# Kernel optimization log

Measured on AMD Instinct MI355X. Metric: run time of the kernel, lower is better.

## Reference

```python
import jax, jax.numpy as jnp
import numpy as np

B, T = 2048, 2048
VOCAB, E, H = 32000, 4, 4


def _gru_layer(x, Wih, Whh, bih, bhh, reverse=False):
    """PyTorch-semantics GRU over batch_first x [B,T,F]; returns [B,T,H]."""
    Bn = x.shape[0]
    Hn = Whh.shape[1]
    # Precompute input projections for all timesteps: [B,T,3H]
    xi = jnp.einsum('btf,gf->btg', x, Wih) + bih
    if reverse:
        xi = xi[:, ::-1]
    xi_t = jnp.swapaxes(xi, 0, 1)  # [T,B,3H]

    def step(h, xt):
        gh = h @ Whh.T + bhh                      # [B,3H]
        xr, xz, xn = jnp.split(xt, 3, axis=-1)
        hr, hz, hn = jnp.split(gh, 3, axis=-1)
        r = jax.nn.sigmoid(xr + hr)
        z = jax.nn.sigmoid(xz + hz)
        n = jnp.tanh(xn + r * hn)
        h_new = (1.0 - z) * n + z * h
        return h_new, h_new

    h0 = jnp.zeros((Bn, Hn), x.dtype)
    _, ys = jax.lax.scan(step, h0, xi_t)
    ys = jnp.swapaxes(ys, 0, 1)  # [B,T,H]
    if reverse:
        ys = ys[:, ::-1]
    return ys


def setup_inputs() -> dict:
    key = jax.random.key(0)
    ks = jax.random.split(key, 16)
    x = jax.random.randint(ks[0], (B, T), 0, VOCAB, dtype=jnp.int64)
    s = 0.3  # xavier-ish scale for tiny dims
    emb   = jax.random.normal(ks[1], (VOCAB, E), jnp.float32) * s
    Wih_f = jax.random.normal(ks[2], (3 * H, E), jnp.float32) * s
    Whh_f = jax.random.normal(ks[3], (3 * H, H), jnp.float32) * s
    Wih_b = jax.random.normal(ks[4], (3 * H, E), jnp.float32) * s
    Whh_b = jax.random.normal(ks[5], (3 * H, H), jnp.float32) * s
    Wih_o = jax.random.normal(ks[6], (3 * 1, 2 * H), jnp.float32) * s
    Whh_o = jax.random.normal(ks[7], (3 * 1, 1), jnp.float32) * s
    z = jnp.zeros
    return {
        'x': x, 'emb': emb,
        'Wih_f': Wih_f, 'Whh_f': Whh_f, 'bih_f': z((3 * H,)), 'bhh_f': z((3 * H,)),
        'Wih_b': Wih_b, 'Whh_b': Whh_b, 'bih_b': z((3 * H,)), 'bhh_b': z((3 * H,)),
        'Wih_o': Wih_o, 'Whh_o': Whh_o, 'bih_o': z((3,)), 'bhh_o': z((3,)),
    }


def reference(x, emb, Wih_f, Whh_f, bih_f, bhh_f, Wih_b, Whh_b, bih_b, bhh_b,
              Wih_o, Whh_o, bih_o, bhh_o):
    h = emb[x]                                         # [B,T,E]
    fwd = _gru_layer(h, Wih_f, Whh_f, bih_f, bhh_f, reverse=False)
    bwd = _gru_layer(h, Wih_b, Whh_b, bih_b, bhh_b, reverse=True)
    bi = jnp.concatenate([fwd, bwd], axis=-1)          # [B,T,2H]
    out = _gru_layer(bi, Wih_o, Whh_o, bih_o, bhh_o)   # [B,T,1]
    return jax.nn.sigmoid(out).reshape(x.shape[0], -1) # [B,T]
```

## Files before the change

kernel.cpp:

```cpp
#include <hip/hip_runtime.h>
#include <hip/hip_bf16.h>
#include <hip/hip_fp16.h>


#define NB 2048
#define NT 2048
#define NV 32000
#define PA_CH 32
#define PA_CL 64
#define PA_WUP 24
#define PB_CH 64
#define PB_CL 32
#define PB_WUP 16
#define CH 32
#define CL (NT / CH)
#define WUP 64

#define W_EMB    0
#define W_WIH_F  128000
#define W_WHH_F  128048
#define W_BIH_F  128096
#define W_BHH_F  128108
#define W_WIH_B  128120
#define W_WHH_B  128168
#define W_BIH_B  128216
#define W_BHH_B  128228
#define W_WIH_O  128240
#define W_WHH_O  128264
#define W_BIH_O  128267
#define W_BHH_O  128270
#define W_TOTAL  128273

#define XT_PAD 24

static constexpr size_t WBLK_BYTES = 524288;
static constexpr size_t D_BYTES    = (size_t)NT * NB * 8;
static constexpr size_t XT_BYTES_P = (size_t)(NT + 2 * XT_PAD) * NB * 2;
static constexpr size_t XIH_BYTES  = (size_t)NV * 16 * 2;
static constexpr size_t N2_XIH_F   = WBLK_BYTES;
static constexpr size_t N2_XIH_B   = N2_XIH_F + XIH_BYTES;
static constexpr size_t N2_DF      = N2_XIH_B + XIH_BYTES;
static constexpr size_t N2_DB      = N2_DF + D_BYTES;
static constexpr size_t N2_XT      = N2_DB + D_BYTES;
static constexpr size_t NEED_NEW2  = N2_XT + XT_BYTES_P;
static constexpr size_t XI_STRIDE  = 16;
static constexpr size_t XI_BYTES   = (size_t)NV * XI_STRIDE * 4;
static constexpr size_t HS_BYTES   = (size_t)NT * NB * 4 * 2;
static constexpr size_t OFF_XI_F   = WBLK_BYTES;
static constexpr size_t OFF_XI_B   = OFF_XI_F + XI_BYTES;
static constexpr size_t OFF_HS_B   = OFF_XI_B + XI_BYTES;
static constexpr size_t OFF_HS_F   = OFF_HS_B + HS_BYTES;
static constexpr size_t NEED_XI    = OFF_HS_B;
static constexpr size_t NEED_FAST  = OFF_HS_F + HS_BYTES;

#define L2E  1.4426950408889634f
#define L2E2 2.8853900817779268f

typedef __attribute__((ext_vector_type(2))) _Float16 h2v;

__device__ __forceinline__ float frcp_(float x) { return __builtin_amdgcn_rcpf(x); }
__device__ __forceinline__ float sigm_(float x) { return frcp_(1.f + __expf(-x)); }
__device__ __forceinline__ float tanh_(float x) { return 1.f - 2.f * frcp_(1.f + __expf(2.f * x)); }
__device__ __forceinline__ float b2f_(__hip_bfloat16 v) { return __bfloat162float(v); }
__device__ __forceinline__ unsigned f2bf_(float f) {
  __hip_bfloat16 h = __float2bfloat16(f);
  return (unsigned)__builtin_bit_cast(unsigned short, h);
}
__device__ __forceinline__ unsigned pack2_(float a, float b) { return f2bf_(a) | (f2bf_(b) << 16); }
__device__ __forceinline__ float bflo_(unsigned u) { return __builtin_bit_cast(float, u << 16); }
__device__ __forceinline__ float bfhi_(unsigned u) { return __builtin_bit_cast(float, u & 0xffff0000u); }
__device__ __forceinline__ float2 h2f2_(unsigned u) {
  __half2 h = __builtin_bit_cast(__half2, u);
  return __half22float2(h);
}
__device__ __forceinline__ unsigned packh2_(float a, float b) {
  __half2 h = __floats2half2_rn(a, b);
  return __builtin_bit_cast(unsigned, h);
}
__device__ __forceinline__ h2v packh2v_(float a, float b) {
  return __builtin_bit_cast(h2v, packh2_(a, b));
}

#if __has_builtin(__builtin_amdgcn_fdot2)
#define FDOT2_(a, b, c) __builtin_amdgcn_fdot2((a), (b), (c), false)
#else
__device__ __forceinline__ float FDOT2_(h2v a, h2v b, float c) {
  return c + (float)a.x * (float)b.x + (float)a.y * (float)b.y;
}
#endif
#if __has_builtin(__builtin_amdgcn_exp2f)
#define EXP2_(x) __builtin_amdgcn_exp2f(x)
#else
#define EXP2_(x) __expf(0.6931471805599453f * (x))
#endif

__device__ __forceinline__ int probe_is_bf16_(const void* emb) {
  const unsigned short* u = (const unsigned short*)emb;
  int sane = 0;
#pragma unroll
  for (int i = 0; i < 64; ++i) {
    unsigned short v = u[2 * i];
    unsigned e = (v >> 7) & 0xff;
    sane += (e >= 107 && e <= 146) || ((v & 0x7fff) == 0);
  }
  return sane >= 48;
}
__device__ __forceinline__ int probe_x_is64_(const int* x) {
  int zeros = 0;
#pragma unroll
  for (int i = 0; i < 32; ++i) zeros += (x[2 * i + 1] == 0);
  return zeros >= 28;
}
__device__ __forceinline__ int tok_(const int* x, size_t idx, int is64) {
  return is64 ? x[idx * 2] : x[idx];
}
__device__ __forceinline__ float ldf_(const void* p, int i, int isb) {
  return isb ? b2f_(((const __hip_bfloat16*)p)[i]) : ((const float*)p)[i];
}

__global__ void prep_p10(const int* __restrict__ x,
                         const void* emb, const void* Wih_f, const void* Whh_f,
                         const void* bih_f, const void* bhh_f,
                         const void* Wih_b, const void* Whh_b,
                         const void* bih_b, const void* bhh_b,
                         const void* Wih_o, const void* Whh_o,
                         const void* bih_o, const void* bhh_o,
                         __half* __restrict__ xih_f, __half* __restrict__ xih_b,
                         unsigned short* __restrict__ xT, float* __restrict__ W) {
  __shared__ int tile[64][65];
  const int blk = blockIdx.x;
  if (blk < 251) {
    const int tid = blk * 256 + (int)threadIdx.x;
    if (tid >= 2 * NV) return;
    const int isb = probe_is_bf16_(emb);
    const int dir = (tid >= NV) ? 1 : 0;
    const int v = dir ? tid - NV : tid;
    const void* Wih = dir ? Wih_b : Wih_f;
    const void* bih = dir ? bih_b : bih_f;
    const void* bhh = dir ? bhh_b : bhh_f;
    char* dst = (char*)((dir ? xih_b : xih_f) + (size_t)v * 16);
    const float e0 = ldf_(emb, v * 4 + 0, isb), e1 = ldf_(emb, v * 4 + 1, isb);
    const float e2 = ldf_(emb, v * 4 + 2, isb), e3 = ldf_(emb, v * 4 + 3, isb);
    float g[12];
#pragma unroll
    for (int gi = 0; gi < 12; ++gi) {
      float s = ldf_(bih, gi, isb) + (gi < 8 ? ldf_(bhh, gi, isb) : 0.f);
      s += ldf_(Wih, gi * 4 + 0, isb) * e0 + ldf_(Wih, gi * 4 + 1, isb) * e1 +
           ldf_(Wih, gi * 4 + 2, isb) * e2 + ldf_(Wih, gi * 4 + 3, isb) * e3;
      g[gi] = s * (gi < 8 ? L2E : L2E2);
    }
    uint4 qa, qb;
    qa.x = packh2_(g[0], g[1]);  qa.y = packh2_(g[2], g[3]);
    qa.z = packh2_(g[4], g[5]);  qa.w = packh2_(g[6], g[7]);
    qb.x = packh2_(g[8], g[9]);  qb.y = packh2_(g[10], g[11]);
    qb.z = 0u; qb.w = 0u;
    *(uint4*)(dst) = qa;
    *(uint4*)(dst + 16) = qb;
  } else if (blk < 1275) {
    const int x64 = probe_x_is64_(x);
    const int bi2 = blk - 251;
    const int tb = bi2 & 31;
    const int tt = bi2 >> 5;
    const int b0 = tb * 64, t0 = tt * 64;
    const int r = (int)threadIdx.x >> 2;
    const int s = (int)threadIdx.x & 3;
    const int bb = b0 + r;
    if (x64) {
      const uint4* p = (const uint4*)(x + ((size_t)bb * NT + t0 + s * 16) * 2);
#pragma unroll
      for (int i = 0; i < 8; ++i) {
        uint4 q = p[i];
        tile[r][s * 16 + 2 * i] = (int)q.x;
        tile[r][s * 16 + 2 * i + 1] = (int)q.z;
      }
    } else {
      const uint4* p = (const uint4*)(x + (size_t)bb * NT + t0 + s * 16);
#pragma unroll
      for (int i = 0; i < 4; ++i) {
        uint4 q = p[i];
        const int base = s * 16 + 4 * i;
        tile[r][base] = (int)q.x; tile[r][base + 1] = (int)q.y;
        tile[r][base + 2] = (int)q.z; tile[r][base + 3] = (int)q.w;
      }
    }
    __syncthreads();
    const int tx = (int)threadIdx.x & 63, ty = (int)threadIdx.x >> 6;
#pragma unroll
    for (int j = 0; j < 16; ++j) {
      const int t = t0 + ty + 4 * j;
      xT[(size_t)t * NB + b0 + tx] = (unsigned short)tile[tx][ty + 4 * j];
    }
  } else {
    const int i0 = (int)threadIdx.x;
    if (i0 >= W_TOTAL - W_WHH_F) return;
    const int isb = probe_is_bf16_(emb);
    const int i = W_WHH_F + i0;
    const void* src; int off;
    if      (i < W_BIH_F) { src = Whh_f; off = i - W_WHH_F; }
    else if (i < W_BHH_F) { src = bih_f; off = i - W_BIH_F; }
    else if (i < W_WIH_B) { src = bhh_f; off = i - W_BHH_F; }
    else if (i < W_WHH_B) { src = Wih_b; off = i - W_WIH_B; }
    else if (i < W_BIH_B) { src = Whh_b; off = i - W_WHH_B; }
    else if (i < W_BHH_B) { src = bih_b; off = i - W_BIH_B; }
    else if (i < W_WIH_O) { src = bhh_b; off = i - W_BHH_B; }
    else if (i < W_WHH_O) { src = Wih_o; off = i - W_WIH_O; }
    else if (i < W_BIH_O) { src = Whh_o; off = i - W_WHH_O; }
    else if (i < W_BHH_O) { src = bih_o; off = i - W_BIH_O; }
    else                  { src = bhh_o; off = i - W_BHH_O; }
    W[i] = ldf_(src, off, isb);
  }
}

__global__ void __launch_bounds__(64, 2)
gru_scan_p10(const unsigned short* __restrict__ xT, const float* __restrict__ W,
             const __half* __restrict__ xih_f, const __half* __restrict__ xih_b,
             unsigned* __restrict__ df, unsigned* __restrict__ db) {
  const int bi = blockIdx.x;
  const int rg = bi & 31;
  const int c = (bi >> 5) & (PA_CH - 1);
  const int dir = bi >> 10;
  const int b = rg * 64 + (int)threadIdx.x;
  const char* __restrict__ xib = (const char*)(dir ? xih_b : xih_f);
  const char* __restrict__ xtb = (const char*)xT;
  char* __restrict__ dsb = (char*)(dir ? db : df);
  const float* Whh = W + (dir ? W_WHH_B : W_WHH_F);
  const float* bhh = W + (dir ? W_BHH_B : W_BHH_F);

  h2v wh01[12], wh23[12];
#pragma unroll
  for (int g = 0; g < 12; ++g) {
    const float sc = (g < 8) ? L2E : L2E2;
    wh01[g] = packh2v_(Whh[g * 4 + 0] * sc, Whh[g * 4 + 1] * sc);
    wh23[g] = packh2v_(Whh[g * 4 + 2] * sc, Whh[g * 4 + 3] * sc);
  }
  float bn[4];
#pragma unroll
  for (int j = 0; j < 4; ++j) bn[j] = bhh[8 + j] * L2E2;
  h2v wr01 = packh2v_(W[W_WIH_O + dir * 4 + 0] * L2E, W[W_WIH_O + dir * 4 + 1] * L2E);
  h2v wr23 = packh2v_(W[W_WIH_O + dir * 4 + 2] * L2E, W[W_WIH_O + dir * 4 + 3] * L2E);
  h2v wz01 = packh2v_(W[W_WIH_O + 8 + dir * 4 + 0] * L2E, W[W_WIH_O + 8 + dir * 4 + 1] * L2E);
  h2v wz23 = packh2v_(W[W_WIH_O + 8 + dir * 4 + 2] * L2E, W[W_WIH_O + 8 + dir * 4 + 3] * L2E);
  h2v wn01 = packh2v_(W[W_WIH_O + 16 + dir * 4 + 0] * L2E2, W[W_WIH_O + 16 + dir * 4 + 1] * L2E2);
  h2v wn23 = packh2v_(W[W_WIH_O + 16 + dir * 4 + 2] * L2E2, W[W_WIH_O + 16 + dir * 4 + 3] * L2E2);

  const int lo = c * PA_CL, hi = lo + PA_CL;
  int t0, d, wsteps;
  if (dir == 0) {
    d = 1;
    t0 = (c == 0) ? 0 : lo - PA_WUP;
    wsteps = (c == 0) ? 0 : PA_WUP;
  } else {
    d = -1;
    t0 = (c == PA_CH - 1) ? NT - 1 : hi - 1 + PA_WUP;
    wsteps = (c == PA_CH - 1) ? 0 : PA_WUP;
  }

#define CLMP(tt_) ((tt_) < 0 ? 0 : ((tt_) > NT - 1 ? NT - 1 : (tt_)))

  uint4 XA[8], XB[8];
  int KT[8];
#pragma unroll
  for (int j = 0; j < 8; ++j) {
    const int tj = CLMP(t0 + j * d);
    const unsigned kj = (unsigned)xT[(size_t)tj * NB + b] << 5;
    XA[j] = *(const uint4*)(xib + kj);
    XB[j] = *(const uint4*)(xib + kj + 16);
  }
#pragma unroll
  for (int j = 0; j < 8; ++j) {
    const int tj = CLMP(t0 + (8 + j) * d);
    KT[j] = (int)xT[(size_t)tj * NB + b];
  }

  const int dtok = d * (NB * 2);
  int otok = (t0 + 16 * d) * (NB * 2) + b * 2;

  float h[4] = {0.f, 0.f, 0.f, 0.f};
  h2v h01p = packh2v_(0.f, 0.f), h23p = packh2v_(0.f, 0.f);
  int odot = 0;
  const int ddot = d * (NB * 8);

#define ASTEP(J, DO_STORE)                                                     \
  {                                                                            \
    const unsigned ko = (unsigned)KT[J] << 5;                                  \
    const uint4 A = XA[J];                                                     \
    const uint4 Bq = XB[J];                                                    \
    XA[J] = *(const uint4*)(xib + ko);                                         \
    XB[J] = *(const uint4*)(xib + ko + 16);                                    \
    KT[J] = (int)*(const unsigned short*)(xtb + otok);                         \
    otok += dtok;                                                              \
    const float2 r01 = h2f2_(A.x), r23 = h2f2_(A.y);                           \
    const float2 z01 = h2f2_(A.z), z23 = h2f2_(A.w);                           \
    const float2 n01 = h2f2_(Bq.x), n23 = h2f2_(Bq.y);                         \
    const float xr[4] = {r01.x, r01.y, r23.x, r23.y};                          \
    const float xz[4] = {z01.x, z01.y, z23.x, z23.y};                          \
    const float xnn[4] = {n01.x, n01.y, n23.x, n23.y};                         \
    _Pragma("unroll")                                                          \
    for (int j = 0; j < 4; ++j) {                                              \
      const float ar = FDOT2_(wh01[j], h01p, FDOT2_(wh23[j], h23p, xr[j]));    \
      const float az = FDOT2_(wh01[4 + j], h01p,                               \
                              FDOT2_(wh23[4 + j], h23p, xz[j]));               \
      const float an = FDOT2_(wh01[8 + j], h01p,                               \
                              FDOT2_(wh23[8 + j], h23p, bn[j]));               \
      const float rr = frcp_(1.f + EXP2_(-ar));                                \
      const float zz = frcp_(1.f + EXP2_(-az));                                \
      const float q = frcp_(1.f + EXP2_(__builtin_fmaf(rr, an, xnn[j])));      \
      const float n = __builtin_fmaf(-2.f, q, 1.f);                            \
      h[j] = n + zz * (h[j] - n);                                              \
    }                                                                          \
    h01p = packh2v_(h[0], h[1]);                                               \
    h23p = packh2v_(h[2], h[3]);                                               \
    if (DO_STORE) {                                                            \
      const float dr = FDOT2_(wr01, h01p, FDOT2_(wr23, h23p, 0.f));            \
      const float dz = FDOT2_(wz01, h01p, FDOT2_(wz23, h23p, 0.f));            \
      const float dn = FDOT2_(wn01, h01p, FDOT2_(wn23, h23p, 0.f));            \
      uint2 st;                                                                \
      st.x = packh2_(dr, dz);                                                  \
      st.y = packh2_(dn, 0.f);                                                 \
      *(uint2*)(dsb + odot) = st;                                              \
      odot += ddot;                                                            \
    }                                                                          \
  }

  if (wsteps) {
#pragma unroll 1
    for (int i = 0; i < PA_WUP; i += 8) {
      ASTEP(0, 0) ASTEP(1, 0) ASTEP(2, 0) ASTEP(3, 0)
      ASTEP(4, 0) ASTEP(5, 0) ASTEP(6, 0) ASTEP(7, 0)
    }
  }
  {
    const int te = (d > 0) ? lo : hi - 1;
    odot = te * (NB * 8) + b * 8;
  }
#pragma unroll 1
  for (int i = 0; i < PA_CL; i += 8) {
    ASTEP(0, 1) ASTEP(1, 1) ASTEP(2, 1) ASTEP(3, 1)
    ASTEP(4, 1) ASTEP(5, 1) ASTEP(6, 1) ASTEP(7, 1)
  }
#undef ASTEP
#undef CLMP
}

__global__ void __launch_bounds__(64, 2)
out_scan_p10(const unsigned* __restrict__ df, const unsigned* __restrict__ db,
             const float* __restrict__ W, float* __restrict__ out) {
  const int bi = blockIdx.x;
  const int rg = bi & 31;
  const int c = bi >> 5;
  const int b = rg * 64 + (int)threadIdx.x;
  const float ur = W[W_WHH_O + 0] * L2E, uz = W[W_WHH_O + 1] * L2E;
  const float un = W[W_WHH_O + 2] * L2E2;
  const float cr = (W[W_BIH_O + 0] + W[W_BHH_O + 0]) * L2E;
  const float cz = (W[W_BIH_O + 1] + W[W_BHH_O + 1]) * L2E;
  const float cx = W[W_BIH_O + 2] * L2E2;
  const float ch = W[W_BHH_O + 2] * L2E2;
  const char* __restrict__ dfb = (const char*)df;
  const char* __restrict__ dbb = (const char*)db;

  const int lo = c * PB_CL;
  const int t0 = (c == 0) ? 0 : lo - PB_WUP;
  const int wsteps = (c == 0) ? 0 : PB_WUP;

  uint2 F[8], Bv[8];
#pragma unroll
  for (int j = 0; j < 8; ++j) {
    const int off = (t0 + j) * (NB * 8) + b * 8;
    F[j] = *(const uint2*)(dfb + off);
    Bv[j] = *(const uint2*)(dbb + off);
  }
  int ofs = (t0 + 8) * (NB * 8) + b * 8;
  const int ofshi = (NT - 1) * (NB * 8) + b * 8;

  float h = 0.f;
  float ob[PB_CL];

#define BSTEP(S, EMIT, OBI)                                                    \
  {                                                                            \
    const uint2 Fc = F[S], Bc = Bv[S];                                         \
    F[S] = *(const uint2*)(dfb + ofs);                                         \
    Bv[S] = *(const uint2*)(dbb + ofs);                                        \
    ofs += NB * 8;                                                             \
    ofs = ofs > ofshi ? ofshi : ofs;                                           \
    const float2 fa = h2f2_(Fc.x);                                             \
    const float2 fb = h2f2_(Fc.y);                                             \
    const float2 ba = h2f2_(Bc.x);                                             \
    const float2 bb = h2f2_(Bc.y);                                             \
    const float ar = cr + ur * h + fa.x + ba.x;                                \
    const float az = cz + uz * h + fa.y + ba.y;                                \
    const float ax = cx + fb.x + bb.x;                                         \
    const float an = ch + un * h;                                              \
    const float rr = frcp_(1.f + EXP2_(-ar));                                  \
    const float zz = frcp_(1.f + EXP2_(-az));                                  \
    const float q = frcp_(1.f + EXP2_(__builtin_fmaf(rr, an, ax)));            \
    const float nn = __builtin_fmaf(-2.f, q, 1.f);                             \
    h = nn + zz * (h - nn);                                                    \
    if (EMIT) ob[OBI] = sigm_(h);                                              \
  }

  if (wsteps) {
#pragma unroll 1
    for (int i = 0; i < 2; ++i) {
      BSTEP(0, 0, 0) BSTEP(1, 0, 0) BSTEP(2, 0, 0) BSTEP(3, 0, 0)
      BSTEP(4, 0, 0) BSTEP(5, 0, 0) BSTEP(6, 0, 0) BSTEP(7, 0, 0)
    }
  }
  BSTEP(0, 1, 0)  BSTEP(1, 1, 1)  BSTEP(2, 1, 2)  BSTEP(3, 1, 3)
  BSTEP(4, 1, 4)  BSTEP(5, 1, 5)  BSTEP(6, 1, 6)  BSTEP(7, 1, 7)
  BSTEP(0, 1, 8)  BSTEP(1, 1, 9)  BSTEP(2, 1, 10) BSTEP(3, 1, 11)
  BSTEP(4, 1, 12) BSTEP(5, 1, 13) BSTEP(6, 1, 14) BSTEP(7, 1, 15)
  BSTEP(0, 1, 16) BSTEP(1, 1, 17) BSTEP(2, 1, 18) BSTEP(3, 1, 19)
  BSTEP(4, 1, 20) BSTEP(5, 1, 21) BSTEP(6, 1, 22) BSTEP(7, 1, 23)
  BSTEP(0, 1, 24) BSTEP(1, 1, 25) BSTEP(2, 1, 26) BSTEP(3, 1, 27)
  BSTEP(4, 1, 28) BSTEP(5, 1, 29) BSTEP(6, 1, 30) BSTEP(7, 1, 31)
#undef BSTEP

  float* dp = out + (size_t)b * NT + lo;
#pragma unroll
  for (int j = 0; j < 8; ++j) {
    float4 q = {ob[4 * j], ob[4 * j + 1], ob[4 * j + 2], ob[4 * j + 3]};
    *(float4*)(dp + 4 * j) = q;
  }
}

__global__ void convert_weights_kernel(const void* emb, const void* Wih_f, const void* Whh_f,
                                       const void* bih_f, const void* bhh_f,
                                       const void* Wih_b, const void* Whh_b,
                                       const void* bih_b, const void* bhh_b,
                                       const void* Wih_o, const void* Whh_o,
                                       const void* bih_o, const void* bhh_o,
                                       float* __restrict__ W) {
  const int isb = probe_is_bf16_(emb);
  for (int i = blockIdx.x * blockDim.x + threadIdx.x; i < W_TOTAL;
       i += gridDim.x * blockDim.x) {
    const void* src; int off;
    if      (i < W_WIH_F) { src = emb;   off = i; }
    else if (i < W_WHH_F) { src = Wih_f; off = i - W_WIH_F; }
    else if (i < W_BIH_F) { src = Whh_f; off = i - W_WHH_F; }
    else if (i < W_BHH_F) { src = bih_f; off = i - W_BIH_F; }
    else if (i < W_WIH_B) { src = bhh_f; off = i - W_BHH_F; }
    else if (i < W_WHH_B) { src = Wih_b; off = i - W_WIH_B; }
    else if (i < W_BIH_B) { src = Whh_b; off = i - W_WHH_B; }
    else if (i < W_BHH_B) { src = bih_b; off = i - W_BIH_B; }
    else if (i < W_WIH_O) { src = bhh_b; off = i - W_BHH_B; }
    else if (i < W_WHH_O) { src = Wih_o; off = i - W_WIH_O; }
    else if (i < W_BIH_O) { src = Whh_o; off = i - W_WHH_O; }
    else if (i < W_BHH_O) { src = bih_o; off = i - W_BIH_O; }
    else                  { src = bhh_o; off = i - W_BHH_O; }
    W[i] = ldf_(src, off, isb);
  }
}

__global__ void build_xi_kernel(const float* __restrict__ W,
                                float* __restrict__ xi_f, float* __restrict__ xi_b) {
  const int tid = blockIdx.x * blockDim.x + threadIdx.x;
  if (tid >= 2 * NV) return;
  const int dir = (tid >= NV) ? 1 : 0;
  const int v = dir ? tid - NV : tid;
  const float* Wih = W + (dir ? W_WIH_B : W_WIH_F);
  const float* bih = W + (dir ? W_BIH_B : W_BIH_F);
  const float* bhh = W + (dir ? W_BHH_B : W_BHH_F);
  float* dstp = (dir ? xi_b : xi_f) + (size_t)v * XI_STRIDE;
  const float e0 = W[W_EMB + v * 4 + 0], e1 = W[W_EMB + v * 4 + 1];
  const float e2 = W[W_EMB + v * 4 + 2], e3 = W[W_EMB + v * 4 + 3];
#pragma unroll
  for (int g = 0; g < 12; ++g) {
    float s = bih[g] + (g < 8 ? bhh[g] : 0.f);
    s += Wih[g * 4 + 0] * e0 + Wih[g * 4 + 1] * e1 + Wih[g * 4 + 2] * e2 + Wih[g * 4 + 3] * e3;
    dstp[g] = s;
  }
}

__global__ void __launch_bounds__(64, 1)
gru_scan_chunked(const int* __restrict__ x, const float* __restrict__ W,
                 const float* __restrict__ xi_f, const float* __restrict__ xi_b,
                 unsigned* __restrict__ hs_f, unsigned* __restrict__ hs_b) {
  const int bi = blockIdx.x;
  const int rg = bi & 31;
  const int c = (bi >> 5) & (CH - 1);
  const int dir = bi / (32 * CH);
  const int b = rg * 64 + (int)threadIdx.x;
  const int x64 = probe_x_is64_(x);
  const float* __restrict__ xi = dir ? xi_b : xi_f;
  const float* Whh = W + (dir ? W_WHH_B : W_WHH_F);
  const float* bhh = W + (dir ? W_BHH_B : W_BHH_F);
  unsigned* __restrict__ hs = dir ? hs_b : hs_f;
  float w[12][4];
#pragma unroll
  for (int g = 0; g < 12; ++g)
#pragma unroll
    for (int k = 0; k < 4; ++k) w[g][k] = Whh[g * 4 + k];
  float bn[4];
#pragma unroll
  for (int j = 0; j < 4; ++j) bn[j] = bhh[8 + j];
  const size_t xbase = (size_t)b * NT;
  const int lo = c * CL, hi = lo + CL;
  int t0, d, nsteps, tlast;
  if (dir == 0) {
    t0 = lo - WUP; if (t0 < 0) t0 = 0;
    d = 1; nsteps = hi - t0; tlast = hi - 1;
  } else {
    t0 = hi - 1 + WUP; if (t0 > NT - 1) t0 = NT - 1;
    d = -1; nsteps = t0 - lo + 1; tlast = lo;
  }
  int k2;
  float4 X0a, X0b, X0c, X1a, X1b, X1c;
  {
    int tb = t0 + d;     if (d > 0) { if (tb > tlast) tb = tlast; } else { if (tb < tlast) tb = tlast; }
    int tc = t0 + 2 * d; if (d > 0) { if (tc > tlast) tc = tlast; } else { if (tc < tlast) tc = tlast; }
    const int ka = tok_(x, xbase + t0, x64);
    const int kb = tok_(x, xbase + tb, x64);
    k2 = tok_(x, xbase + tc, x64);
    const float4* p = (const float4*)(xi + (size_t)ka * XI_STRIDE);
    X0a = p[0]; X0b = p[1]; X0c = p[2];
    const float4* q = (const float4*)(xi + (size_t)kb * XI_STRIDE);
    X1a = q[0]; X1b = q[1]; X1c = q[2];
  }
  float h[4] = {0.f, 0.f, 0.f, 0.f};
  int t = t0;
  for (int i = 0; i < nsteps; ++i) {
    int td = t + 3 * d; if (d > 0) { if (td > tlast) td = tlast; } else { if (td < tlast) td = tlast; }
    const int k3 = tok_(x, xbase + td, x64);
    const float4* p2 = (const float4*)(xi + (size_t)k2 * XI_STRIDE);
    float4 X2a = p2[0], X2b = p2[1], X2c = p2[2];
    const float xr[4] = {X0a.x, X0a.y, X0a.z, X0a.w};
    const float xz[4] = {X0b.x, X0b.y, X0b.z, X0b.w};
    const float xn[4] = {X0c.x, X0c.y, X0c.z, X0c.w};
    float r[4], z[4], n[4];
#pragma unroll
    for (int j = 0; j < 4; ++j) {
      float ar = xr[j], az = xz[j], an = bn[j];
#pragma unroll
      for (int k = 0; k < 4; ++k) {
        ar += w[j][k] * h[k];
        az += w[4 + j][k] * h[k];
        an += w[8 + j][k] * h[k];
      }
      r[j] = sigm_(ar); z[j] = sigm_(az); n[j] = tanh_(xn[j] + r[j] * an);
    }
#pragma unroll
    for (int j = 0; j < 4; ++j) h[j] = n[j] + z[j] * (h[j] - n[j]);
    if ((unsigned)(t - lo) < (unsigned)CL) {
      const size_t idx = ((size_t)t * NB + b) * 2;
      uint2 st; st.x = pack2_(h[0], h[1]); st.y = pack2_(h[2], h[3]);
      *(uint2*)(hs + idx) = st;
    }
    X0a = X1a; X0b = X1b; X0c = X1c;
    X1a = X2a; X1b = X2b; X1c = X2c;
    k2 = k3; t += d;
  }
}

__global__ void __launch_bounds__(64, 1)
out_scan_chunked(const unsigned* __restrict__ hs_f, const unsigned* __restrict__ hs_b,
                 const float* __restrict__ W, float* __restrict__ out) {
  const int bi = blockIdx.x;
  const int rg = bi & 31;
  const int c = bi >> 5;
  const int b = rg * 64 + (int)threadIdx.x;
  float wr[8], wz[8], wn[8];
#pragma unroll
  for (int k = 0; k < 8; ++k) {
    wr[k] = W[W_WIH_O + k]; wz[k] = W[W_WIH_O + 8 + k]; wn[k] = W[W_WIH_O + 16 + k];
  }
  const float ur = W[W_WHH_O + 0], uz = W[W_WHH_O + 1], un = W[W_WHH_O + 2];
  const float cr = W[W_BIH_O + 0] + W[W_BHH_O + 0];
  const float cz = W[W_BIH_O + 1] + W[W_BHH_O + 1];
  const float cx = W[W_BIH_O + 2];
  const float ch = W[W_BHH_O + 2];
  const int lo = c * CL, hi = lo + CL;
  int t0 = lo - WUP; if (t0 < 0) t0 = 0;
  float h = 0.f;
  uint2 F0, Bb0, F1, Bb1;
  {
    const size_t i0 = ((size_t)t0 * NB + b) * 2;
    F0 = *(const uint2*)(hs_f + i0); Bb0 = *(const uint2*)(hs_b + i0);
    int t1 = t0 + 1; if (t1 > hi - 1) t1 = hi - 1;
    const size_t i1 = ((size_t)t1 * NB + b) * 2;
    F1 = *(const uint2*)(hs_f + i1); Bb1 = *(const uint2*)(hs_b + i1);
  }
  float ob[8];
  for (int t = t0; t < hi; ++t) {
    int tp = t + 2; if (tp > hi - 1) tp = hi - 1;
    const size_t ip = ((size_t)tp * NB + b) * 2;
    uint2 F2 = *(const uint2*)(hs_f + ip);
    uint2 Bb2 = *(const uint2*)(hs_b + ip);
    const float bi8[8] = {bflo_(F0.x), bfhi_(F0.x), bflo_(F0.y), bfhi_(F0.y),
                          bflo_(Bb0.x), bfhi_(Bb0.x), bflo_(Bb0.y), bfhi_(Bb0.y)};
    float ar = cr + ur * h, az = cz + uz * h, an = ch + un * h, ax = cx;
#pragma unroll
    for (int k = 0; k < 8; ++k) {
      ar += wr[k] * bi8[k]; az += wz[k] * bi8[k]; ax += wn[k] * bi8[k];
    }
    const float r = sigm_(ar), z = sigm_(az);
    const float n = tanh_(ax + r * an);
    h = n + z * (h - n);
    if (t >= lo) {
      ob[t & 7] = sigm_(h);
      if ((t & 7) == 7) {
        float4 q0 = {ob[0], ob[1], ob[2], ob[3]};
        float4 q1 = {ob[4], ob[5], ob[6], ob[7]};
        float4* dstp = (float4*)(out + (size_t)b * NT + (t & ~7));
        dstp[0] = q0; dstp[1] = q1;
      }
    }
    F0 = F1; Bb0 = Bb1; F1 = F2; Bb1 = Bb2;
  }
}

__global__ void __launch_bounds__(64, 1)
fwd_out_scan_kernel(const int* __restrict__ x, const float* __restrict__ W,
                    const float* __restrict__ xi_f, const unsigned* __restrict__ hs_b,
                    float* __restrict__ out) {
  const int b = blockIdx.x * 64 + threadIdx.x;
  const int x64 = probe_x_is64_(x);
  float w[12][4];
#pragma unroll
  for (int g = 0; g < 12; ++g)
#pragma unroll
    for (int k = 0; k < 4; ++k) w[g][k] = W[W_WHH_F + g * 4 + k];
  float bn[4];
#pragma unroll
  for (int j = 0; j < 4; ++j) bn[j] = W[W_BHH_F + 8 + j];
  float wr[8], wz[8], wno[8];
#pragma unroll
  for (int k = 0; k < 8; ++k) {
    wr[k] = W[W_WIH_O + k]; wz[k] = W[W_WIH_O + 8 + k]; wno[k] = W[W_WIH_O + 16 + k];
  }
  const float ur = W[W_WHH_O + 0], uz = W[W_WHH_O + 1], un = W[W_WHH_O + 2];
  const float cr = W[W_BIH_O + 0] + W[W_BHH_O + 0];
  const float cz = W[W_BIH_O + 1] + W[W_BHH_O + 1];
  const float cx = W[W_BIH_O + 2];
  const float chh = W[W_BHH_O + 2];
  const size_t xbase = (size_t)b * NT;
  float h[4] = {0.f, 0.f, 0.f, 0.f};
  float ho = 0.f;
  const float4* p0 = (const float4*)(xi_f + (size_t)tok_(x, xbase, x64) * XI_STRIDE);
  float4 A0 = p0[0], A1 = p0[1], A2 = p0[2];
  for (int tg = 0; tg < NT / 8; ++tg) {
    float ob[8];
#pragma unroll
    for (int s = 0; s < 8; ++s) {
      const int t = tg * 8 + s;
      const int tn = (t + 1 < NT) ? t + 1 : t;
      const float4* pn = (const float4*)(xi_f + (size_t)tok_(x, xbase + tn, x64) * XI_STRIDE);
      float4 B0 = pn[0], B1 = pn[1], B2 = pn[2];
      const size_t idx = ((size_t)t * NB + b) * 2;
      uint2 ub = {0u, 0u};
      if (hs_b) ub = *(const uint2*)(hs_b + idx);
      const float xr[4] = {A0.x, A0.y, A0.z, A0.w};
      const float xz[4] = {A1.x, A1.y, A1.z, A1.w};
      const float xn[4] = {A2.x, A2.y, A2.z, A2.w};
      float r[4], z[4], n[4];
#pragma unroll
      for (int j = 0; j < 4; ++j) {
        float ar = xr[j], az = xz[j], an = bn[j];
#pragma unroll
        for (int k = 0; k < 4; ++k) {
          ar += w[j][k] * h[k]; az += w[4 + j][k] * h[k]; an += w[8 + j][k] * h[k];
        }
        r[j] = sigm_(ar); z[j] = sigm_(az); n[j] = tanh_(xn[j] + r[j] * an);
      }
#pragma unroll
      for (int j = 0; j < 4; ++j) h[j] = n[j] + z[j] * (h[j] - n[j]);
      const float bi8[8] = {h[0], h[1], h[2], h[3],
                            bflo_(ub.x), bfhi_(ub.x), bflo_(ub.y), bfhi_(ub.y)};
      float ar = cr + ur * ho, az = cz + uz * ho, an = chh + un * ho, ax = cx;
#pragma unroll
      for (int k = 0; k < 8; ++k) {
        ar += wr[k] * bi8[k]; az += wz[k] * bi8[k]; ax += wno[k] * bi8[k];
      }
      const float rr = sigm_(ar), zz = sigm_(az);
      const float nn = tanh_(ax + rr * an);
      ho = nn + zz * (ho - nn);
      ob[s] = sigm_(ho);
      A0 = B0; A1 = B1; A2 = B2;
    }
    float4 q0 = {ob[0], ob[1], ob[2], ob[3]};
    float4 q1 = {ob[4], ob[5], ob[6], ob[7]};
    float4* dstp = (float4*)(out + (size_t)b * NT + tg * 8);
    dstp[0] = q0; dstp[1] = q1;
  }
}

__global__ void fill_sentinel_kernel(float* out, int n) {
  int i = blockIdx.x * blockDim.x + threadIdx.x;
  if (i < n) out[i] = 0.25f;
}

extern "C" void kernel_launch(void* const* d_in, const int* in_sizes, int n_in,
                              void* d_out, int out_size, void* d_ws, size_t ws_size,
                              hipStream_t stream) {
  (void)in_sizes; (void)n_in;
  const int* x = (const int*)d_in[0];
  char* ws = (char*)d_ws;
  float* W = (float*)ws;
  float* out = (float*)d_out;

  if (ws_size < NEED_XI) {
    fill_sentinel_kernel<<<(out_size + 255) / 256, 256, 0, stream>>>(out, out_size);
    return;
  }

  if (ws_size >= NEED_NEW2) {
    __half* xih_f = (__half*)(ws + N2_XIH_F);
    __half* xih_b = (__half*)(ws + N2_XIH_B);
    unsigned* df = (unsigned*)(ws + N2_DF);
    unsigned* db = (unsigned*)(ws + N2_DB);
    unsigned short* xT_alloc = (unsigned short*)(ws + N2_XT);
    unsigned short* xT = xT_alloc + (size_t)XT_PAD * NB;
    prep_p10<<<1276, 256, 0, stream>>>(
        x, d_in[1], d_in[2], d_in[3], d_in[4], d_in[5], d_in[6], d_in[7],
        d_in[8], d_in[9], d_in[10], d_in[11], d_in[12], d_in[13],
        xih_f, xih_b, xT, W);
    gru_scan_p10<<<2 * PA_CH * 32, 64, 0, stream>>>(xT, W, xih_f, xih_b, df, db);
    out_scan_p10<<<PB_CH * 32, 64, 0, stream>>>(df, db, W, out);
    return;
  }

  convert_weights_kernel<<<504, 256, 0, stream>>>(
      d_in[1], d_in[2], d_in[3], d_in[4], d_in[5], d_in[6], d_in[7],
      d_in[8], d_in[9], d_in[10], d_in[11], d_in[12], d_in[13], W);
  float* xi_f = (float*)(ws + OFF_XI_F);
  float* xi_b = (float*)(ws + OFF_XI_B);
  unsigned* hs_b = (unsigned*)(ws + OFF_HS_B);
  unsigned* hs_f = (unsigned*)(ws + OFF_HS_F);
  build_xi_kernel<<<(2 * NV + 255) / 256, 256, 0, stream>>>(W, xi_f, xi_b);
  if (ws_size >= NEED_FAST) {
    gru_scan_chunked<<<2 * CH * 32, 64, 0, stream>>>(x, W, xi_f, xi_b, hs_f, hs_b);
    out_scan_chunked<<<CH * 32, 64, 0, stream>>>(hs_f, hs_b, W, out);
  } else {
    fwd_out_scan_kernel<<<NB / 64, 64, 0, stream>>>(x, W, xi_f, nullptr, out);
  }
}
```

Baseline: 107.4 us.

## Interleave two independent batch rows per thread and halve time chunk length in GRU scan

Each thread now advances two independent batch rows (b and b+1024) in the same loop, giving the scheduler two independent dependency chains to hide latency of the serial recurrence. Chunks are halved to 32 timesteps with 64 chunks, keeping the total block count the same, while warmup stays at 24 steps. This cuts per-thread serial length but raises warmup overhead relative to useful work and raises register pressure, with the prefetch depth reduced from 8 to 4 per row.

```diff
diff --git a/kernel.cpp b/kernel.cpp
--- a/kernel.cpp
+++ b/kernel.cpp
@@ -6,9 +6,9 @@
 #define NB 2048
 #define NT 2048
 #define NV 32000
-#define PA_CH 32
-#define PA_CL 64
-#define PA_WUP 24
+#define PA2_CH 64
+#define PA2_CL 32
+#define PA2_WUP 24
 #define PB_CH 64
 #define PB_CL 32
 #define PB_WUP 16
@@ -212,12 +212,12 @@
 }
 
 __global__ void __launch_bounds__(64, 2)
-gru_scan_p10(const unsigned short* __restrict__ xT, const float* __restrict__ W,
+gru_scan_p11(const unsigned short* __restrict__ xT, const float* __restrict__ W,
              const __half* __restrict__ xih_f, const __half* __restrict__ xih_b,
              unsigned* __restrict__ df, unsigned* __restrict__ db) {
   const int bi = blockIdx.x;
-  const int rg = bi & 31;
-  const int c = (bi >> 5) & (PA_CH - 1);
+  const int rg = bi & 15;
+  const int c = (bi >> 4) & (PA2_CH - 1);
   const int dir = bi >> 10;
   const int b = rg * 64 + (int)threadIdx.x;
   const char* __restrict__ xib = (const char*)(dir ? xih_b : xih_f);
@@ -243,90 +243,109 @@
   h2v wn01 = packh2v_(W[W_WIH_O + 16 + dir * 4 + 0] * L2E2, W[W_WIH_O + 16 + dir * 4 + 1] * L2E2);
   h2v wn23 = packh2v_(W[W_WIH_O + 16 + dir * 4 + 2] * L2E2, W[W_WIH_O + 16 + dir * 4 + 3] * L2E2);
 
-  const int lo = c * PA_CL, hi = lo + PA_CL;
+  const int lo = c * PA2_CL, hi = lo + PA2_CL;
   int t0, d, wsteps;
   if (dir == 0) {
     d = 1;
-    t0 = (c == 0) ? 0 : lo - PA_WUP;
-    wsteps = (c == 0) ? 0 : PA_WUP;
+    t0 = (c == 0) ? 0 : lo - PA2_WUP;
+    wsteps = (c == 0) ? 0 : PA2_WUP;
   } else {
     d = -1;
-    t0 = (c == PA_CH - 1) ? NT - 1 : hi - 1 + PA_WUP;
-    wsteps = (c == PA_CH - 1) ? 0 : PA_WUP;
+    t0 = (c == PA2_CH - 1) ? NT - 1 : hi - 1 + PA2_WUP;
+    wsteps = (c == PA2_CH - 1) ? 0 : PA2_WUP;
   }
 
 #define CLMP(tt_) ((tt_) < 0 ? 0 : ((tt_) > NT - 1 ? NT - 1 : (tt_)))
 
-  uint4 XA[8], XB[8];
-  int KT[8];
-#pragma unroll
-  for (int j = 0; j < 8; ++j) {
+  uint4 XA0[4], XB0[4], XA1[4], XB1[4];
+  int KT0[4], KT1[4];
+#pragma unroll
+  for (int j = 0; j < 4; ++j) {
     const int tj = CLMP(t0 + j * d);
-    const unsigned kj = (unsigned)xT[(size_t)tj * NB + b] << 5;
-    XA[j] = *(const uint4*)(xib + kj);
-    XB[j] = *(const uint4*)(xib + kj + 16);
-  }
-#pragma unroll
-  for (int j = 0; j < 8; ++j) {
-    const int tj = CLMP(t0 + (8 + j) * d);
-    KT[j] = (int)xT[(size_t)tj * NB + b];
+    const unsigned k0 = (unsigned)xT[(size_t)tj * NB + b] << 5;
+    const unsigned k1 = (unsigned)xT[(size_t)tj * NB + b + 1024] << 5;
+    XA0[j] = *(const uint4*)(xib + k0);
+    XB0[j] = *(const uint4*)(xib + k0 + 16);
+    XA1[j] = *(const uint4*)(xib + k1);
+    XB1[j] = *(const uint4*)(xib + k1 + 16);
+  }
+#pragma unroll
+  for (int j = 0; j < 4; ++j) {
+    const int tj = CLMP(t0 + (4 + j) * d);
+    KT0[j] = (int)xT[(size_t)tj * NB + b];
+    KT1[j] = (int)xT[(size_t)tj * NB + b + 1024];
   }
 
   const int dtok = d * (NB * 2);
-  int otok = (t0 + 16 * d) * (NB * 2) + b * 2;
-
-  float h[4] = {0.f, 0.f, 0.f, 0.f};
-  h2v h01p = packh2v_(0.f, 0.f), h23p = packh2v_(0.f, 0.f);
+  int otok = (t0 + 8 * d) * (NB * 2) + b * 2;
+
+  float h0[4] = {0.f, 0.f, 0.f, 0.f};
+  float h1[4] = {0.f, 0.f, 0.f, 0.f};
+  h2v h01p0 = packh2v_(0.f, 0.f), h23p0 = packh2v_(0.f, 0.f);
+  h2v h01p1 = packh2v_(0.f, 0.f), h23p1 = packh2v_(0.f, 0.f);
   int odot = 0;
   const int ddot = d * (NB * 8);
 
-#define ASTEP(J, DO_STORE)                                                     \
+#define GMATH(A, Bq, hp01, hp23, h)                                            \
+    {                                                                          \
+      const float2 r01 = h2f2_(A.x), r23 = h2f2_(A.y);                         \
+      const float2 z01 = h2f2_(A.z), z23 = h2f2_(A.w);                         \
+      const float2 n01 = h2f2_(Bq.x), n23 = h2f2_(Bq.y);                       \
+      const float xr[4] = {r01.x, r01.y, r23.x, r23.y};                        \
+      const float xz[4] = {z01.x, z01.y, z23.x, z23.y};                        \
+      const float xnn[4] = {n01.x, n01.y, n23.x, n23.y};                       \
+      _Pragma("unroll")                                                        \
+      for (int j = 0; j < 4; ++j) {                                            \
+        const float ar = FDOT2_(wh01[j], hp01, FDOT2_(wh23[j], hp23, xr[j]));  \
+        const float az = FDOT2_(wh01[4 + j], hp01,                             \
+                                FDOT2_(wh23[4 + j], hp23, xz[j]));             \
+        const float an = FDOT2_(wh01[8 + j], hp01,                             \
+                                FDOT2_(wh23[8 + j], hp23, bn[j]));             \
+        const float rr = frcp_(1.f + EXP2_(-ar));                              \
+        const float zz = frcp_(1.f + EXP2_(-az));                              \
+        const float q = frcp_(1.f + EXP2_(__builtin_fmaf(rr, an, xnn[j])));    \
+        const float n = __builtin_fmaf(-2.f, q, 1.f);                          \
+        h[j] = n + zz * (h[j] - n);                                            \
+      }                                                                        \
+      hp01 = packh2v_(h[0], h[1]);                                             \
+      hp23 = packh2v_(h[2], h[3]);                                             \
+    }
+
+#define ASTEP2(J, DO_STORE)                                                    \
   {                                                                            \
-    const unsigned ko = (unsigned)KT[J] << 5;                                  \
-    const uint4 A = XA[J];                                                     \
-    const uint4 Bq = XB[J];                                                    \
-    XA[J] = *(const uint4*)(xib + ko);                                         \
-    XB[J] = *(const uint4*)(xib + ko + 16);                                    \
-    KT[J] = (int)*(const unsigned short*)(xtb + otok);                         \
+    const unsigned ko0 = (unsigned)KT0[J] << 5;                                \
+    const unsigned ko1 = (unsigned)KT1[J] << 5;                                \
+    const uint4 A0 = XA0[J], B0q = XB0[J];                                     \
+    const uint4 A1 = XA1[J], B1q = XB1[J];                                     \
+    XA0[J] = *(const uint4*)(xib + ko0);                                       \
+    XB0[J] = *(const uint4*)(xib + ko0 + 16);                                  \
+    XA1[J] = *(const uint4*)(xib + ko1);                                       \
+    XB1[J] = *(const uint4*)(xib + ko1 + 16);                                  \
+    KT0[J] = (int)*(const unsigned short*)(xtb + otok);                        \
+    KT1[J] = (int)*(const unsigned short*)(xtb + otok + 2048);                 \
     otok += dtok;                                                              \
-    const float2 r01 = h2f2_(A.x), r23 = h2f2_(A.y);                           \
-    const float2 z01 = h2f2_(A.z), z23 = h2f2_(A.w);                           \
-    const float2 n01 = h2f2_(Bq.x), n23 = h2f2_(Bq.y);                         \
-    const float xr[4] = {r01.x, r01.y, r23.x, r23.y};                          \
-    const float xz[4] = {z01.x, z01.y, z23.x, z23.y};                          \
-    const float xnn[4] = {n01.x, n01.y, n23.x, n23.y};                         \
-    _Pragma("unroll")                                                          \
-    for (int j = 0; j < 4; ++j) {                                              \
-      const float ar = FDOT2_(wh01[j], h01p, FDOT2_(wh23[j], h23p, xr[j]));    \
-      const float az = FDOT2_(wh01[4 + j], h01p,                               \
-                              FDOT2_(wh23[4 + j], h23p, xz[j]));               \
-      const float an = FDOT2_(wh01[8 + j], h01p,                               \
-                              FDOT2_(wh23[8 + j], h23p, bn[j]));               \
-      const float rr = frcp_(1.f + EXP2_(-ar));                                \
-      const float zz = frcp_(1.f + EXP2_(-az));                                \
-      const float q = frcp_(1.f + EXP2_(__builtin_fmaf(rr, an, xnn[j])));      \
-      const float n = __builtin_fmaf(-2.f, q, 1.f);                            \
-      h[j] = n + zz * (h[j] - n);                                              \
-    }                                                                          \
-    h01p = packh2v_(h[0], h[1]);                                               \
-    h23p = packh2v_(h[2], h[3]);                                               \
+    GMATH(A0, B0q, h01p0, h23p0, h0)                                           \
+    GMATH(A1, B1q, h01p1, h23p1, h1)                                           \
     if (DO_STORE) {                                                            \
-      const float dr = FDOT2_(wr01, h01p, FDOT2_(wr23, h23p, 0.f));            \
-      const float dz = FDOT2_(wz01, h01p, FDOT2_(wz23, h23p, 0.f));            \
-      const float dn = FDOT2_(wn01, h01p, FDOT2_(wn23, h23p, 0.f));            \
-      uint2 st;                                                                \
-      st.x = packh2_(dr, dz);                                                  \
-      st.y = packh2_(dn, 0.f);                                                 \
-      *(uint2*)(dsb + odot) = st;                                              \
+      const float dr0 = FDOT2_(wr01, h01p0, FDOT2_(wr23, h23p0, 0.f));         \
+      const float dz0 = FDOT2_(wz01, h01p0, FDOT2_(wz23, h23p0, 0.f));         \
+      const float dn0 = FDOT2_(wn01, h01p0, FDOT2_(wn23, h23p0, 0.f));         \
+      const float dr1 = FDOT2_(wr01, h01p1, FDOT2_(wr23, h23p1, 0.f));         \
+      const float dz1 = FDOT2_(wz01, h01p1, FDOT2_(wz23, h23p1, 0.f));         \
+      const float dn1 = FDOT2_(wn01, h01p1, FDOT2_(wn23, h23p1, 0.f));         \
+      uint2 st0, st1;                                                          \
+      st0.x = packh2_(dr0, dz0);  st0.y = packh2_(dn0, 0.f);                   \
+      st1.x = packh2_(dr1, dz1);  st1.y = packh2_(dn1, 0.f);                   \
+      *(uint2*)(dsb + odot) = st0;                                             \
+      *(uint2*)(dsb + odot + 8192) = st1;                                      \
       odot += ddot;                                                            \
     }                                                                          \
   }
 
   if (wsteps) {
 #pragma unroll 1
-    for (int i = 0; i < PA_WUP; i += 8) {
-      ASTEP(0, 0) ASTEP(1, 0) ASTEP(2, 0) ASTEP(3, 0)
-      ASTEP(4, 0) ASTEP(5, 0) ASTEP(6, 0) ASTEP(7, 0)
+    for (int i = 0; i < PA2_WUP; i += 4) {
+      ASTEP2(0, 0) ASTEP2(1, 0) ASTEP2(2, 0) ASTEP2(3, 0)
     }
   }
   {
@@ -334,11 +353,11 @@
     odot = te * (NB * 8) + b * 8;
   }
 #pragma unroll 1
-  for (int i = 0; i < PA_CL; i += 8) {
-    ASTEP(0, 1) ASTEP(1, 1) ASTEP(2, 1) ASTEP(3, 1)
-    ASTEP(4, 1) ASTEP(5, 1) ASTEP(6, 1) ASTEP(7, 1)
-  }
-#undef ASTEP
+  for (int i = 0; i < PA2_CL; i += 4) {
+    ASTEP2(0, 1) ASTEP2(1, 1) ASTEP2(2, 1) ASTEP2(3, 1)
+  }
+#undef ASTEP2
+#undef GMATH
 #undef CLMP
 }
 
@@ -713,7 +732,7 @@
         x, d_in[1], d_in[2], d_in[3], d_in[4], d_in[5], d_in[6], d_in[7],
         d_in[8], d_in[9], d_in[10], d_in[11], d_in[12], d_in[13],
         xih_f, xih_b, xT, W);
-    gru_scan_p10<<<2 * PA_CH * 32, 64, 0, stream>>>(xT, W, xih_f, xih_b, df, db);
+    gru_scan_p11<<<2 * PA2_CH * 16, 64, 0, stream>>>(xT, W, xih_f, xih_b, df, db);
     out_scan_p10<<<PB_CH * 32, 64, 0, stream>>>(df, db, W, out);
     return;
   }
```

After: 124.7 us, median of 2. +16.1%, slower.
